# Performance work log

Measured on AMD Instinct MI355X. Metric: run time of the kernel, lower is better.

Reference implementation:

```python
import jax, jax.numpy as jnp
import numpy as np

B, N, D = 4, 4096, 1024
H, S, R = 16, 256, 2           # heads, segment size, dilation rate
DH = D // H
LN_EPS = 1e-5


def _hilbert_perm(n_side):
    # perm[d] = linear index (y*side + x) of the d-th point on the Hilbert curve
    def d2xy(n, d):
        x = y = 0
        t = d
        s = 1
        while s < n:
            rx = 1 & (t // 2)
            ry = 1 & (t ^ rx)
            if ry == 0:
                if rx == 1:
                    x = s - 1 - x
                    y = s - 1 - y
                x, y = y, x
            x += s * rx
            y += s * ry
            t //= 4
            s *= 2
        return x, y
    perm = np.empty(n_side * n_side, dtype=np.int32)
    for d in range(n_side * n_side):
        xx, yy = d2xy(n_side, d)
        perm[d] = yy * n_side + xx
    return perm


def setup_inputs() -> dict:
    key = jax.random.key(0)
    ks = jax.random.split(key, 8)
    sc = 0.02
    return {
        "x": jax.random.normal(ks[0], (B, N, D), jnp.float32),
        "ln1_g": jnp.ones((D,), jnp.float32),
        "ln1_b": jnp.zeros((D,), jnp.float32),
        "w_qkv": jax.random.normal(ks[1], (D, 3 * D), jnp.float32) * sc,
        "b_qkv": jnp.zeros((3 * D,), jnp.float32),
        "w_o": jax.random.normal(ks[2], (D, D), jnp.float32) * sc,
        "b_o": jnp.zeros((D,), jnp.float32),
        "ln2_g": jnp.ones((D,), jnp.float32),
        "ln2_b": jnp.zeros((D,), jnp.float32),
        "w1": jax.random.normal(ks[3], (D, 4 * D), jnp.float32) * sc,
        "b1": jnp.zeros((4 * D,), jnp.float32),
        "w2": jax.random.normal(ks[4], (4 * D, D), jnp.float32) * sc,
        "b2": jnp.zeros((D,), jnp.float32),
        "hilbert_perm": jnp.asarray(_hilbert_perm(int(np.sqrt(N)))),
    }


def _layernorm(x, g, b):
    mu = jnp.mean(x, axis=-1, keepdims=True)
    var = jnp.mean(jnp.square(x - mu), axis=-1, keepdims=True)
    return (x - mu) * jax.lax.rsqrt(var + LN_EPS) * g + b


def _hilbert_dilated_attention(x, w_qkv, b_qkv, w_o, b_o, perm):
    b, n, d = x.shape
    nseg, sr = n // S, S // R
    xp = jnp.take(x, perm, axis=1)                    # Hilbert reorder
    qkv = xp @ w_qkv + b_qkv                          # [b,n,3d]
    q, k, v = jnp.split(qkv, 3, axis=-1)
    def seg(t):
        return t.reshape(b, nseg, S, H, DH)
    q, k, v = seg(q), seg(k), seg(v)
    # per-head dilation offset: head h attends positions (h % R) :: R in each segment
    offs = jnp.arange(H, dtype=jnp.int32) % R                        # [H]
    idx = offs[None, :] + R * jnp.arange(sr, dtype=jnp.int32)[:, None]  # [sr,H]
    idx_g = idx[None, None, :, :, None]                              # [1,1,sr,H,1]
    qd = jnp.take_along_axis(q, idx_g, axis=2)        # [b,nseg,sr,H,dh]
    kd = jnp.take_along_axis(k, idx_g, axis=2)
    vd = jnp.take_along_axis(v, idx_g, axis=2)
    scores = jnp.einsum('bgqhd,bgkhd->bghqk', qd, kd) / jnp.sqrt(jnp.asarray(DH, x.dtype))
    attn = jax.nn.softmax(scores, axis=-1)
    od = jnp.einsum('bghqk,bgkhd->bgqhd', attn, vd)   # [b,nseg,sr,H,dh]
    # scatter back into full segments; uncovered (head,pos) slots stay zero
    out = jnp.zeros((b, nseg, S, H, DH), x.dtype)
    out = out.at[:, :, idx, jnp.arange(H)[None, :], :].set(od)
    out = out.reshape(b, n, d) @ w_o + b_o
    inv = jnp.argsort(perm)
    return jnp.take(out, inv, axis=1)                 # inverse Hilbert reorder


def reference(x, ln1_g, ln1_b, w_qkv, b_qkv, w_o, b_o, ln2_g, ln2_b, w1, b1, w2, b2, hilbert_perm):
    h = _layernorm(x, ln1_g, ln1_b)
    h = _hilbert_dilated_attention(h, w_qkv, b_qkv, w_o, b_o, hilbert_perm)
    x = x + h
    h = _layernorm(x, ln2_g, ln2_b)
    h = jax.nn.gelu(h @ w1 + b1, approximate=False) @ w2 + b2
    return x + h
```

## Files before the change

### kernel.cpp

```cpp
#include <hip/hip_runtime.h>

typedef short bf16x8 __attribute__((ext_vector_type(8)));
typedef float f32x4 __attribute__((ext_vector_type(4)));
typedef unsigned short u16;

#define GLDS16(g, l) __builtin_amdgcn_global_load_lds( \
    (const __attribute__((address_space(1))) void*)(g), \
    (__attribute__((address_space(3))) void*)(l), 16, 0, 0)

#define DSR_(dst, p) asm volatile("ds_read_b128 %0, %1" \
    : "=v"(dst) : "v"((const __attribute__((address_space(3))) void*)(p)))

__device__ __forceinline__ u16 f2b(float f) {
  unsigned u = __float_as_uint(f);
  u += 0x7fffu + ((u >> 16) & 1u);
  return (u16)(u >> 16);
}

__global__ __launch_bounds__(256)
void transpose_bf16(const float* __restrict__ w, u16* __restrict__ wt, int K, int N) {
  __shared__ float tile[32][33];
  const int n0 = blockIdx.x * 32, k0 = blockIdx.y * 32;
  const int tx = threadIdx.x & 31, ty = threadIdx.x >> 5;
#pragma unroll
  for (int i = 0; i < 4; ++i)
    tile[ty + i * 8][tx] = w[(size_t)(k0 + ty + i * 8) * N + n0 + tx];
  __syncthreads();
#pragma unroll
  for (int i = 0; i < 4; ++i)
    wt[(size_t)(n0 + ty + i * 8) * K + k0 + tx] = f2b(tile[tx][ty + i * 8]);
}

__global__ __launch_bounds__(256)
void ln_rows(const float* __restrict__ src, const float* __restrict__ gam,
             const float* __restrict__ bet, const int* __restrict__ perm,
             u16* __restrict__ dst) {
  const int orow = blockIdx.x;
  const int b = orow >> 12, j = orow & 4095;
  const int srow = perm ? ((b << 12) + perm[j]) : orow;
  const float4 v = ((const float4*)(src + (size_t)srow * 1024))[threadIdx.x];
  float s = v.x + v.y + v.z + v.w;
  float s2 = v.x * v.x + v.y * v.y + v.z * v.z + v.w * v.w;
#pragma unroll
  for (int d = 1; d < 64; d <<= 1) { s += __shfl_xor(s, d); s2 += __shfl_xor(s2, d); }
  __shared__ float rs[4], rs2[4];
  const int wave = threadIdx.x >> 6, lane = threadIdx.x & 63;
  if (lane == 0) { rs[wave] = s; rs2[wave] = s2; }
  __syncthreads();
  s = rs[0] + rs[1] + rs[2] + rs[3];
  s2 = rs2[0] + rs2[1] + rs2[2] + rs2[3];
  const float mu = s * (1.f / 1024.f);
  const float var = s2 * (1.f / 1024.f) - mu * mu;
  const float rstd = rsqrtf(var + 1e-5f);
  const int c = threadIdx.x * 4;
  const float4 gg = *(const float4*)(gam + c);
  const float4 bb = *(const float4*)(bet + c);
  const u16 o0 = f2b((v.x - mu) * rstd * gg.x + bb.x);
  const u16 o1 = f2b((v.y - mu) * rstd * gg.y + bb.y);
  const u16 o2 = f2b((v.z - mu) * rstd * gg.z + bb.z);
  const u16 o3 = f2b((v.w - mu) * rstd * gg.w + bb.w);
  const unsigned lo = (unsigned)o0 | ((unsigned)o1 << 16);
  const unsigned hi = (unsigned)o2 | ((unsigned)o3 << 16);
  *(uint2*)(dst + (size_t)orow * 1024 + c) = make_uint2(lo, hi);
}

template <int EPI>
__global__ __launch_bounds__(512, 2)
void gemm256(const u16* __restrict__ A, const u16* __restrict__ Bt,
             const float* __restrict__ bias, void* __restrict__ Cout,
             const float* __restrict__ resid, const int* __restrict__ perm,
             int M, int Nn, int K) {
  __shared__ u16 sm[65536];
  char* const smc = (char*)sm;
  const int tid = threadIdx.x;
  const int w = tid >> 6, lane = tid & 63;
  const int lr = lane & 15, lg = lane >> 4;
  const int wm = w >> 2, wn = w & 3;

  const int wg = blockIdx.x;
  const int x = wg & 7, l = wg >> 3;
  const int mm = (l >> 2) & 7, nn = l & 3, ng = l >> 5;
  const int m0 = ((x << 3) + mm) << 8;
  const int n0 = ((ng << 2) + nn) << 8;

  const int srow = tid >> 3;
  const int scol = ((tid & 7) ^ (srow & 7)) << 3;
  const size_t aSrc = (size_t)(m0 + srow) * K + scol;
  const size_t bSrc = (size_t)(n0 + srow) * K + scol;
  char* const lWav = smc + w * 1024;

  const int slot0 = (lg ^ (lr & 7)) << 4;
  const int aRow = (wm * 128 + lr) * 128;
  const int bRow = (wn * 64 + lr) * 128 + 32768;

  const int NT = K >> 6;

#define STAGE_(d, mat, h, k0) do { \
    const u16* gp = ((mat) ? Bt : A) + ((mat) ? bSrc : aSrc) + (size_t)(h) * 128 * K + (k0); \
    char* lp = lWav + (d) * 65536 + (mat) * 32768 + (h) * 16384; \
    GLDS16(gp, lp); GLDS16(gp + (size_t)64 * K, lp + 8192); } while (0)

  bf16x8 aLo[8], aHi[8], bLo[4], bHi[4];

#define R_ALO(P) do { _Pragma("unroll") for (int mf = 0; mf < 4; ++mf) \
    _Pragma("unroll") for (int kk = 0; kk < 2; ++kk) \
      DSR_(aLo[mf * 2 + kk], (P) + mf * 2048 + (slot0 ^ (kk << 6))); } while (0)
#define R_AHI(P) do { _Pragma("unroll") for (int mf = 0; mf < 4; ++mf) \
    _Pragma("unroll") for (int kk = 0; kk < 2; ++kk) \
      DSR_(aHi[mf * 2 + kk], (P) + (4 + mf) * 2048 + (slot0 ^ (kk << 6))); } while (0)
#define R_BLO(P) do { _Pragma("unroll") for (int nf = 0; nf < 2; ++nf) \
    _Pragma("unroll") for (int kk = 0; kk < 2; ++kk) \
      DSR_(bLo[nf * 2 + kk], (P) + nf * 2048 + (slot0 ^ (kk << 6))); } while (0)
#define R_BHI(P) do { _Pragma("unroll") for (int nf = 0; nf < 2; ++nf) \
    _Pragma("unroll") for (int kk = 0; kk < 2; ++kk) \
      DSR_(bHi[nf * 2 + kk], (P) + (2 + nf) * 2048 + (slot0 ^ (kk << 6))); } while (0)

#define QUAD_(AARR, BARR, MB, NB) do { _Pragma("unroll") for (int mf = 0; mf < 4; ++mf) \
    _Pragma("unroll") for (int nf = 0; nf < 2; ++nf) \
    _Pragma("unroll") for (int kk = 0; kk < 2; ++kk) \
      acc[(MB) * 4 + mf][(NB) * 2 + nf] = __builtin_amdgcn_mfma_f32_16x16x32_bf16( \
          AARR[mf * 2 + kk], BARR[nf * 2 + kk], acc[(MB) * 4 + mf][(NB) * 2 + nf], 0, 0, 0); } while (0)

#define LGKM0SB_() do { asm volatile("s_waitcnt lgkmcnt(0)" ::: "memory"); \
                        __builtin_amdgcn_sched_barrier(0); } while (0)

  STAGE_(0, 1, 0, 0); STAGE_(0, 1, 1, 0); STAGE_(0, 0, 0, 0); STAGE_(0, 0, 1, 0);
  if (NT > 1) {
    STAGE_(1, 1, 0, 64); STAGE_(1, 1, 1, 64); STAGE_(1, 0, 0, 64); STAGE_(1, 0, 1, 64);
    asm volatile("s_waitcnt vmcnt(8)" ::: "memory");
  } else {
    asm volatile("s_waitcnt vmcnt(0)" ::: "memory");
  }
  __builtin_amdgcn_s_barrier();

  f32x4 acc[8][4] = {};

  for (int t = 0; t < NT; ++t) {
    const int c = t & 1;
    const char* cA = smc + c * 65536 + aRow;
    const char* cB = smc + c * 65536 + bRow;
    const int k2 = (t + 2) << 6;

    R_ALO(cA); R_BLO(cB);
    LGKM0SB_();
    __builtin_amdgcn_s_setprio(1);
    QUAD_(aLo, bLo, 0, 0);
    __builtin_amdgcn_s_setprio(0);
    R_BHI(cB);
    LGKM0SB_();
    __builtin_amdgcn_s_setprio(1);
    QUAD_(aLo, bHi, 0, 1);
    __builtin_amdgcn_s_setprio(0);
    __builtin_amdgcn_s_barrier();

    if (t + 2 < NT) { STAGE_(c, 1, 0, k2); STAGE_(c, 1, 1, k2); }
    R_AHI(cA);
    LGKM0SB_();
    __builtin_amdgcn_s_setprio(1);
    QUAD_(aHi, bLo, 1, 0);
    __builtin_amdgcn_s_setprio(0);
    __builtin_amdgcn_s_barrier();

    if (t + 2 < NT) { STAGE_(c, 0, 0, k2); STAGE_(c, 0, 1, k2); }
    __builtin_amdgcn_s_setprio(1);
    QUAD_(aHi, bHi, 1, 1);
    __builtin_amdgcn_s_setprio(0);
    if (t < NT - 2) asm volatile("s_waitcnt vmcnt(6)" ::: "memory");
    else            asm volatile("s_waitcnt vmcnt(0)" ::: "memory");
    __builtin_amdgcn_s_barrier();
  }
#undef STAGE_
#undef R_ALO
#undef R_AHI
#undef R_BLO
#undef R_BHI
#undef QUAD_
#undef LGKM0SB_

#pragma unroll
  for (int mf = 0; mf < 8; ++mf) {
#pragma unroll
    for (int nf = 0; nf < 4; ++nf) {
      const int col = n0 + wn * 64 + nf * 16 + lr;
      const float bia = bias[col];
#pragma unroll
      for (int r = 0; r < 4; ++r) {
        const int row = m0 + wm * 128 + mf * 16 + lg * 4 + r;
        float v = acc[mf][nf][r] + bia;
        if (EPI == 0) {
          ((u16*)Cout)[(size_t)row * Nn + col] = f2b(v);
        } else if (EPI == 1) {
          v = 0.5f * v * (1.f + erff(v * 0.70710678118654752f));
          ((u16*)Cout)[(size_t)row * Nn + col] = f2b(v);
        } else if (EPI == 2) {
          const int b = row >> 12, j = row & 4095;
          const size_t di = ((size_t)((b << 12) + perm[j])) * 1024 + col;
          ((float*)Cout)[di] = resid[di] + v;
        } else {
          const size_t di = (size_t)row * 1024 + col;
          ((float*)Cout)[di] = resid[di] + v;
        }
      }
    }
  }
}

__global__ __launch_bounds__(256, 2)
void attn_kernel(const u16* __restrict__ qkv, u16* __restrict__ outp) {
  const int blk = blockIdx.x;
  const int h = blk & 15, g = (blk >> 4) & 15, b = blk >> 8;
  const int tid = threadIdx.x, wave = tid >> 6, lane = tid & 63;
  const int lr = lane & 15, lg = lane >> 4;
  const int par = h & 1;

  __shared__ u16 lQ[128 * 64];
  __shared__ u16 lK[128 * 64];
  __shared__ u16 lVt[64 * 128];
  __shared__ u16 lP[4][32 * 128];

  const size_t rbase = (size_t)((b << 12) + (g << 8) + par);

#pragma unroll
  for (int i = 0; i < 4; ++i) {
    const int ou = i * 4096 + wave * 1024;
    const int o = ou + lane * 16;
    const int j = o >> 7, cb = o & 127;
    const u16* gq = qkv + (rbase + 2 * j) * 3072 + h * 64 + (cb >> 1);
    GLDS16(gq, (char*)lQ + ou);
    GLDS16(gq + 1024, (char*)lK + ou);
  }
#pragma unroll
  for (int i = 0; i < 4; ++i) {
    const int c = tid + i * 256;
    const int j = c >> 3, dc = c & 7;
    const uint4 vv = *(const uint4*)(qkv + (rbase + 2 * j) * 3072 + 2048 + h * 64 + dc * 8);
    const u16* pv = (const u16*)&vv;
#pragma unroll
    for (int e = 0; e < 8; ++e) lVt[(dc * 8 + e) * 128 + j] = pv[e];
  }
  __syncthreads();

  f32x4 sacc[2][8] = {};
#pragma unroll
  for (int kk = 0; kk < 2; ++kk) {
    bf16x8 aq[2], bk[8];
#pragma unroll
    for (int mf = 0; mf < 2; ++mf)
      aq[mf] = *(const bf16x8*)&lQ[(wave * 32 + mf * 16 + lr) * 64 + kk * 32 + lg * 8];
#pragma unroll
    for (int nf = 0; nf < 8; ++nf)
      bk[nf] = *(const bf16x8*)&lK[(nf * 16 + lr) * 64 + kk * 32 + lg * 8];
#pragma unroll
    for (int mf = 0; mf < 2; ++mf)
#pragma unroll
      for (int nf = 0; nf < 8; ++nf)
        sacc[mf][nf] = __builtin_amdgcn_mfma_f32_16x16x32_bf16(aq[mf], bk[nf], sacc[mf][nf], 0, 0, 0);
  }

#pragma unroll
  for (int mf = 0; mf < 2; ++mf) {
#pragma unroll
    for (int r = 0; r < 4; ++r) {
      float mx = -3e38f;
#pragma unroll
      for (int nf = 0; nf < 8; ++nf) mx = fmaxf(mx, sacc[mf][nf][r]);
#pragma unroll
      for (int d = 1; d < 16; d <<= 1) mx = fmaxf(mx, __shfl_xor(mx, d));
      float pv[8];
      float sum = 0.f;
#pragma unroll
      for (int nf = 0; nf < 8; ++nf) {
        pv[nf] = __expf((sacc[mf][nf][r] - mx) * 0.125f);
        sum += pv[nf];
      }
#pragma unroll
      for (int d = 1; d < 16; d <<= 1) sum += __shfl_xor(sum, d);
      const float inv = 1.f / sum;
      const int rrow = mf * 16 + lg * 4 + r;
#pragma unroll
      for (int nf = 0; nf < 8; ++nf)
        lP[wave][rrow * 128 + nf * 16 + lr] = f2b(pv[nf] * inv);
    }
  }
  __syncthreads();

  f32x4 oacc[2][4] = {};
#pragma unroll
  for (int kk = 0; kk < 4; ++kk) {
    bf16x8 ap[2], bv[4];
#pragma unroll
    for (int mf = 0; mf < 2; ++mf)
      ap[mf] = *(const bf16x8*)&lP[wave][(mf * 16 + lr) * 128 + kk * 32 + lg * 8];
#pragma unroll
    for (int nf = 0; nf < 4; ++nf)
      bv[nf] = *(const bf16x8*)&lVt[(nf * 16 + lr) * 128 + kk * 32 + lg * 8];
#pragma unroll
    for (int mf = 0; mf < 2; ++mf)
#pragma unroll
      for (int nf = 0; nf < 4; ++nf)
        oacc[mf][nf] = __builtin_amdgcn_mfma_f32_16x16x32_bf16(ap[mf], bv[nf], oacc[mf][nf], 0, 0, 0);
  }

  u16* obase = outp + ((size_t)((b << 12) + (g << 8))) * 1024 + h * 64;
#pragma unroll
  for (int mf = 0; mf < 2; ++mf)
#pragma unroll
    for (int nf = 0; nf < 4; ++nf)
#pragma unroll
      for (int r = 0; r < 4; ++r) {
        const int jq = wave * 32 + mf * 16 + lg * 4 + r;
        obase[(size_t)(par + 2 * jq) * 1024 + nf * 16 + lr] = f2b(oacc[mf][nf][r]);
      }
  const int jz = tid >> 1, hh = (tid & 1) * 32;
  u16* zp = obase + (size_t)((1 - par) + 2 * jz) * 1024 + hh;
  const uint4 z = make_uint4(0u, 0u, 0u, 0u);
#pragma unroll
  for (int i = 0; i < 4; ++i) ((uint4*)zp)[i] = z;
}

extern "C" void kernel_launch(void* const* d_in, const int* in_sizes, int n_in,
                              void* d_out, int out_size, void* d_ws, size_t ws_size,
                              hipStream_t stream) {
  const float* x    = (const float*)d_in[0];
  const float* ln1g = (const float*)d_in[1];
  const float* ln1b = (const float*)d_in[2];
  const float* wqkv = (const float*)d_in[3];
  const float* bqkv = (const float*)d_in[4];
  const float* wo   = (const float*)d_in[5];
  const float* bo   = (const float*)d_in[6];
  const float* ln2g = (const float*)d_in[7];
  const float* ln2b = (const float*)d_in[8];
  const float* w1   = (const float*)d_in[9];
  const float* b1   = (const float*)d_in[10];
  const float* w2   = (const float*)d_in[11];
  const float* b2   = (const float*)d_in[12];
  const int*   perm = (const int*)d_in[13];
  float* out = (float*)d_out;
  char* ws = (char*)d_ws;

  u16*  r0    = (u16*)ws;
  u16*  qkv   = (u16*)(ws + (32ull << 20));
  u16*  a1    = (u16*)(ws + (32ull << 20));
  float* x2   = (float*)(ws + (160ull << 20));
  u16*  wqkvT = (u16*)(ws + (224ull << 20));
  u16*  woT   = (u16*)(ws + (230ull << 20));
  u16*  w1T   = (u16*)(ws + (232ull << 20));
  u16*  w2T   = (u16*)(ws + (240ull << 20));

  transpose_bf16<<<dim3(3072 / 32, 1024 / 32), 256, 0, stream>>>(wqkv, wqkvT, 1024, 3072);
  transpose_bf16<<<dim3(1024 / 32, 1024 / 32), 256, 0, stream>>>(wo, woT, 1024, 1024);
  transpose_bf16<<<dim3(4096 / 32, 1024 / 32), 256, 0, stream>>>(w1, w1T, 1024, 4096);
  transpose_bf16<<<dim3(1024 / 32, 4096 / 32), 256, 0, stream>>>(w2, w2T, 4096, 1024);

  ln_rows<<<16384, 256, 0, stream>>>(x, ln1g, ln1b, perm, r0);
  gemm256<0><<<(16384 / 256) * (3072 / 256), 512, 0, stream>>>(r0, wqkvT, bqkv, qkv, nullptr, nullptr,
                                                               16384, 3072, 1024);
  attn_kernel<<<1024, 256, 0, stream>>>(qkv, r0);
  gemm256<2><<<(16384 / 256) * (1024 / 256), 512, 0, stream>>>(r0, woT, bo, x2, x, perm,
                                                               16384, 1024, 1024);
  ln_rows<<<16384, 256, 0, stream>>>(x2, ln2g, ln2b, nullptr, r0);
  gemm256<1><<<(16384 / 256) * (4096 / 256), 512, 0, stream>>>(r0, w1T, b1, a1, nullptr, nullptr,
                                                               16384, 4096, 1024);
  gemm256<3><<<(16384 / 256) * (1024 / 256), 512, 0, stream>>>(a1, w2T, b2, out, x2, nullptr,
                                                               16384, 1024, 4096);
}
```

Before: 608.8 us.

## Compute QKV and output projection only for dilation-covered rows and head columns

Exploits the dilation structure: each head only attends to rows of one parity, so the QKV GEMM is split by parity and computes only the rows and head columns actually used. Weights are repacked into parity-specific layouts. The output projection contracts only over the non-zero head half, which removes zero-filling of the attention output. This halves the FLOPs of the QKV and W_o GEMMs, at the cost of more complex indexing, strided A reads and a changed vmcnt wait count.

New measurement: 531.2 us. 12.8% less time.

```diff
diff --git a/kernel.cpp b/kernel.cpp
--- a/kernel.cpp
+++ b/kernel.cpp
@@ -29,6 +29,43 @@
 #pragma unroll
   for (int i = 0; i < 4; ++i)
     wt[(size_t)(n0 + ty + i * 8) * K + k0 + tx] = f2b(tile[tx][ty + i * 8]);
+}
+
+__global__ __launch_bounds__(256)
+void transpose_qkv_pack(const float* __restrict__ w, u16* __restrict__ wp) {
+  __shared__ float tile[32][33];
+  const int n0 = blockIdx.x * 32, k0 = blockIdx.y * 32;
+  const int tx = threadIdx.x & 31, ty = threadIdx.x >> 5;
+#pragma unroll
+  for (int i = 0; i < 4; ++i)
+    tile[ty + i * 8][tx] = w[(size_t)(k0 + ty + i * 8) * 3072 + n0 + tx];
+  __syncthreads();
+#pragma unroll
+  for (int i = 0; i < 4; ++i) {
+    const int col = n0 + ty + i * 8;
+    const int q = (col >> 6) & 1;
+    const int np = (col >> 10) * 512 + ((col >> 7) & 7) * 64 + (col & 63);
+    wp[(size_t)q * (1536 * 1024) + (size_t)np * 1024 + k0 + tx] = f2b(tile[tx][ty + i * 8]);
+  }
+}
+
+__global__ __launch_bounds__(256)
+void transpose_wo_pack(const float* __restrict__ w, u16* __restrict__ wp) {
+  __shared__ float tile[32][33];
+  const int n0 = blockIdx.x * 32, k0 = blockIdx.y * 32;
+  const int tx = threadIdx.x & 31, ty = threadIdx.x >> 5;
+#pragma unroll
+  for (int i = 0; i < 4; ++i)
+    tile[ty + i * 8][tx] = w[(size_t)(k0 + ty + i * 8) * 1024 + n0 + tx];
+  __syncthreads();
+#pragma unroll
+  for (int i = 0; i < 4; ++i) {
+    const int n = n0 + ty + i * 8;
+    const int k = k0 + tx;
+    const int q = (k >> 6) & 1;
+    const int kp = (k >> 7) * 64 + (k & 63);
+    wp[(size_t)q * (1024 * 512) + (size_t)n * 512 + kp] = f2b(tile[tx][ty + i * 8]);
+  }
 }
 
 __global__ __launch_bounds__(256)
@@ -64,12 +101,13 @@
   *(uint2*)(dst + (size_t)orow * 1024 + c) = make_uint2(lo, hi);
 }
 
-template <int EPI>
+template <int EPI, int PAR>
 __global__ __launch_bounds__(512, 2)
 void gemm256(const u16* __restrict__ A, const u16* __restrict__ Bt,
              const float* __restrict__ bias, void* __restrict__ Cout,
              const float* __restrict__ resid, const int* __restrict__ perm,
-             int M, int Nn, int K) {
+             int M, int Nn, int K, int aRS,
+             long aParOff, long bParOff, long cParOff) {
   __shared__ u16 sm[65536];
   char* const smc = (char*)sm;
   const int tid = threadIdx.x;
@@ -77,16 +115,19 @@
   const int lr = lane & 15, lg = lane >> 4;
   const int wm = w >> 2, wn = w & 3;
 
-  const int wg = blockIdx.x;
+  int wg = blockIdx.x;
+  int par = 0;
+  if (PAR) { par = wg & 1; wg >>= 1; }
   const int x = wg & 7, l = wg >> 3;
-  const int mm = (l >> 2) & 7, nn = l & 3, ng = l >> 5;
-  const int m0 = ((x << 3) + mm) << 8;
-  const int n0 = ((ng << 2) + nn) << 8;
+  const int band = (M >> 8) >> 3;
+  const int mm = l % band, nn = l / band;
+  const int m0 = (x * band + mm) << 8;
+  const int n0 = nn << 8;
 
   const int srow = tid >> 3;
   const int scol = ((tid & 7) ^ (srow & 7)) << 3;
-  const size_t aSrc = (size_t)(m0 + srow) * K + scol;
-  const size_t bSrc = (size_t)(n0 + srow) * K + scol;
+  const size_t aSrc = (size_t)(m0 + srow) * aRS + (PAR ? (size_t)par * aParOff : 0) + scol;
+  const size_t bSrc = (size_t)(n0 + srow) * K + (PAR ? (size_t)par * bParOff : 0) + scol;
   char* const lWav = smc + w * 1024;
 
   const int slot0 = (lg ^ (lr & 7)) << 4;
@@ -96,9 +137,10 @@
   const int NT = K >> 6;
 
 #define STAGE_(d, mat, h, k0) do { \
-    const u16* gp = ((mat) ? Bt : A) + ((mat) ? bSrc : aSrc) + (size_t)(h) * 128 * K + (k0); \
+    const size_t rs_ = (mat) ? (size_t)K : (size_t)aRS; \
+    const u16* gp = ((mat) ? Bt : A) + ((mat) ? bSrc : aSrc) + (size_t)(h) * 128 * rs_ + (k0); \
     char* lp = lWav + (d) * 65536 + (mat) * 32768 + (h) * 16384; \
-    GLDS16(gp, lp); GLDS16(gp + (size_t)64 * K, lp + 8192); } while (0)
+    GLDS16(gp, lp); GLDS16(gp + 64 * rs_, lp + 8192); } while (0)
 
   bf16x8 aLo[8], aHi[8], bLo[4], bHi[4];
 
@@ -165,7 +207,7 @@
     __builtin_amdgcn_s_setprio(1);
     QUAD_(aHi, bHi, 1, 1);
     __builtin_amdgcn_s_setprio(0);
-    if (t < NT - 2) asm volatile("s_waitcnt vmcnt(6)" ::: "memory");
+    if (t < NT - 2) asm volatile("s_waitcnt vmcnt(8)" ::: "memory");
     else            asm volatile("s_waitcnt vmcnt(0)" ::: "memory");
     __builtin_amdgcn_s_barrier();
   }
@@ -182,19 +224,26 @@
 #pragma unroll
     for (int nf = 0; nf < 4; ++nf) {
       const int col = n0 + wn * 64 + nf * 16 + lr;
-      const float bia = bias[col];
+      float bia;
+      if (PAR && EPI == 0) {
+        const int s = col >> 9, hh2 = (col >> 6) & 7, d = col & 63;
+        bia = bias[s * 1024 + hh2 * 128 + par * 64 + d];
+      } else {
+        bia = bias[col];
+      }
 #pragma unroll
       for (int r = 0; r < 4; ++r) {
         const int row = m0 + wm * 128 + mf * 16 + lg * 4 + r;
         float v = acc[mf][nf][r] + bia;
         if (EPI == 0) {
-          ((u16*)Cout)[(size_t)row * Nn + col] = f2b(v);
+          ((u16*)Cout)[(PAR ? (size_t)par * cParOff : 0) + (size_t)row * Nn + col] = f2b(v);
         } else if (EPI == 1) {
           v = 0.5f * v * (1.f + erff(v * 0.70710678118654752f));
           ((u16*)Cout)[(size_t)row * Nn + col] = f2b(v);
         } else if (EPI == 2) {
-          const int b = row >> 12, j = row & 4095;
-          const size_t di = ((size_t)((b << 12) + perm[j])) * 1024 + col;
+          const int orig = PAR ? (2 * row + par) : row;
+          const int b2 = orig >> 12, jj = orig & 4095;
+          const size_t di = ((size_t)((b2 << 12) + perm[jj])) * 1024 + col;
           ((float*)Cout)[di] = resid[di] + v;
         } else {
           const size_t di = (size_t)row * 1024 + col;
@@ -206,34 +255,36 @@
 }
 
 __global__ __launch_bounds__(256, 2)
-void attn_kernel(const u16* __restrict__ qkv, u16* __restrict__ outp) {
+void attn_kernel(const u16* __restrict__ qkvp, u16* __restrict__ op) {
   const int blk = blockIdx.x;
   const int h = blk & 15, g = (blk >> 4) & 15, b = blk >> 8;
   const int tid = threadIdx.x, wave = tid >> 6, lane = tid & 63;
   const int lr = lane & 15, lg = lane >> 4;
-  const int par = h & 1;
+  const int par = h & 1, hh = h >> 1;
 
   __shared__ u16 lQ[128 * 64];
   __shared__ u16 lK[128 * 64];
   __shared__ u16 lVt[64 * 128];
   __shared__ u16 lP[4][32 * 128];
 
-  const size_t rbase = (size_t)((b << 12) + (g << 8) + par);
+  const u16* qp = qkvp + (size_t)par * (8192 * 1536);
+  u16* opb = op + (size_t)par * (8192 * 512);
+  const int rbase = (b << 11) + (g << 7);
 
 #pragma unroll
   for (int i = 0; i < 4; ++i) {
     const int ou = i * 4096 + wave * 1024;
     const int o = ou + lane * 16;
     const int j = o >> 7, cb = o & 127;
-    const u16* gq = qkv + (rbase + 2 * j) * 3072 + h * 64 + (cb >> 1);
+    const u16* gq = qp + (size_t)(rbase + j) * 1536 + hh * 64 + (cb >> 1);
     GLDS16(gq, (char*)lQ + ou);
-    GLDS16(gq + 1024, (char*)lK + ou);
+    GLDS16(gq + 512, (char*)lK + ou);
   }
 #pragma unroll
   for (int i = 0; i < 4; ++i) {
     const int c = tid + i * 256;
     const int j = c >> 3, dc = c & 7;
-    const uint4 vv = *(const uint4*)(qkv + (rbase + 2 * j) * 3072 + 2048 + h * 64 + dc * 8);
+    const uint4 vv = *(const uint4*)(qp + (size_t)(rbase + j) * 1536 + 1024 + hh * 64 + dc * 8);
     const u16* pv = (const u16*)&vv;
 #pragma unroll
     for (int e = 0; e < 8; ++e) lVt[(dc * 8 + e) * 128 + j] = pv[e];
@@ -301,7 +352,7 @@
         oacc[mf][nf] = __builtin_amdgcn_mfma_f32_16x16x32_bf16(ap[mf], bv[nf], oacc[mf][nf], 0, 0, 0);
   }
 
-  u16* obase = outp + ((size_t)((b << 12) + (g << 8))) * 1024 + h * 64;
+  u16* obase = opb + (size_t)rbase * 512 + hh * 64;
 #pragma unroll
   for (int mf = 0; mf < 2; ++mf)
 #pragma unroll
@@ -309,13 +360,8 @@
 #pragma unroll
       for (int r = 0; r < 4; ++r) {
         const int jq = wave * 32 + mf * 16 + lg * 4 + r;
-        obase[(size_t)(par + 2 * jq) * 1024 + nf * 16 + lr] = f2b(oacc[mf][nf][r]);
+        obase[(size_t)jq * 512 + nf * 16 + lr] = f2b(oacc[mf][nf][r]);
       }
-  const int jz = tid >> 1, hh = (tid & 1) * 32;
-  u16* zp = obase + (size_t)((1 - par) + 2 * jz) * 1024 + hh;
-  const uint4 z = make_uint4(0u, 0u, 0u, 0u);
-#pragma unroll
-  for (int i = 0; i < 4; ++i) ((uint4*)zp)[i] = z;
 }
 
 extern "C" void kernel_launch(void* const* d_in, const int* in_sizes, int n_in,
@@ -339,28 +385,31 @@
   char* ws = (char*)d_ws;
 
   u16*  r0    = (u16*)ws;
-  u16*  qkv   = (u16*)(ws + (32ull << 20));
+  u16*  qkvp  = (u16*)(ws + (32ull << 20));
+  u16*  op    = (u16*)(ws + (80ull << 20));
   u16*  a1    = (u16*)(ws + (32ull << 20));
   float* x2   = (float*)(ws + (160ull << 20));
-  u16*  wqkvT = (u16*)(ws + (224ull << 20));
-  u16*  woT   = (u16*)(ws + (230ull << 20));
+  u16*  wqkvP = (u16*)(ws + (224ull << 20));
+  u16*  woP   = (u16*)(ws + (230ull << 20));
   u16*  w1T   = (u16*)(ws + (232ull << 20));
   u16*  w2T   = (u16*)(ws + (240ull << 20));
 
-  transpose_bf16<<<dim3(3072 / 32, 1024 / 32), 256, 0, stream>>>(wqkv, wqkvT, 1024, 3072);
-  transpose_bf16<<<dim3(1024 / 32, 1024 / 32), 256, 0, stream>>>(wo, woT, 1024, 1024);
+  transpose_qkv_pack<<<dim3(96, 32), 256, 0, stream>>>(wqkv, wqkvP);
+  transpose_wo_pack<<<dim3(32, 32), 256, 0, stream>>>(wo, woP);
   transpose_bf16<<<dim3(4096 / 32, 1024 / 32), 256, 0, stream>>>(w1, w1T, 1024, 4096);
   transpose_bf16<<<dim3(1024 / 32, 4096 / 32), 256, 0, stream>>>(w2, w2T, 4096, 1024);
 
   ln_rows<<<16384, 256, 0, stream>>>(x, ln1g, ln1b, perm, r0);
-  gemm256<0><<<(16384 / 256) * (3072 / 256), 512, 0, stream>>>(r0, wqkvT, bqkv, qkv, nullptr, nullptr,
-                                                               16384, 3072, 1024);
-  attn_kernel<<<1024, 256, 0, stream>>>(qkv, r0);
-  gemm256<2><<<(16384 / 256) * (1024 / 256), 512, 0, stream>>>(r0, woT, bo, x2, x, perm,
-                                                               16384, 1024, 1024);
+  gemm256<0, 1><<<384, 512, 0, stream>>>(r0, wqkvP, bqkv, qkvp, nullptr, nullptr,
+                                         8192, 1536, 1024, 2048,
+                                         1024L, 1536L * 1024, 8192L * 1536);
+  attn_kernel<<<1024, 256, 0, stream>>>(qkvp, op);
+  gemm256<2, 1><<<256, 512, 0, stream>>>(op, woP, bo, x2, x, perm,
+                                         8192, 1024, 512, 512,
+                                         8192L * 512, 1024L * 512, 0);
   ln_rows<<<16384, 256, 0, stream>>>(x2, ln2g, ln2b, nullptr, r0);
-  gemm256<1><<<(16384 / 256) * (4096 / 256), 512, 0, stream>>>(r0, w1T, b1, a1, nullptr, nullptr,
-                                                               16384, 4096, 1024);
-  gemm256<3><<<(16384 / 256) * (1024 / 256), 512, 0, stream>>>(a1, w2T, b2, out, x2, nullptr,
-                                                               16384, 1024, 4096);
-}
+  gemm256<1, 0><<<1024, 512, 0, stream>>>(r0, w1T, b1, a1, nullptr, nullptr,
+                                          16384, 4096, 1024, 1024, 0, 0, 0);
+  gemm256<3, 0><<<256, 512, 0, stream>>>(a1, w2T, b2, out, x2, nullptr,
+                                         16384, 1024, 4096, 4096, 0, 0, 0);
+}
```
